# Kernel optimization log

Measured on AMD Instinct MI355X. Metric: run time of the kernel, lower is better.

## Reference

```python
import jax, jax.numpy as jnp
import numpy as np

D_MODEL = 512
NUM_HEADS = 8
DEPTH = D_MODEL // NUM_HEADS


def setup_inputs() -> dict:
    key = jax.random.key(0)
    ks = jax.random.split(key, 12)
    B, S, D = 2, 4096, D_MODEL
    scale = 1.0 / np.sqrt(D)
    return {
        "q": jax.random.normal(ks[0], (B, S, D), jnp.float32),
        "k": jax.random.normal(ks[1], (B, S, D), jnp.float32),
        "v": jax.random.normal(ks[2], (B, S, D), jnp.float32),
        "mask": jnp.zeros((B, 1, 1, S), jnp.float32),
        "wq": jax.random.normal(ks[3], (D, D), jnp.float32) * scale,
        "bq": jnp.zeros((D,), jnp.float32),
        "wk": jax.random.normal(ks[4], (D, D), jnp.float32) * scale,
        "bk": jnp.zeros((D,), jnp.float32),
        "wv": jax.random.normal(ks[5], (D, D), jnp.float32) * scale,
        "bv": jnp.zeros((D,), jnp.float32),
        "wo": jax.random.normal(ks[6], (D, D), jnp.float32) * scale,
        "bo": jnp.zeros((D,), jnp.float32),
    }


def _split_heads(x):
    # [B, S, D] -> [B, H, S, depth]
    B, S, _ = x.shape
    return x.reshape(B, S, NUM_HEADS, DEPTH).transpose(0, 2, 1, 3)


def reference(q, k, v, mask, wq, bq, wk, bk, wv, bv, wo, bo):
    B, S, D = q.shape
    query = _split_heads(q @ wq + bq)   # [B,H,S,d]
    key = _split_heads(k @ wk + bk)
    value = _split_heads(v @ wv + bv)
    # NOTE: original module does NOT scale by 1/sqrt(depth)
    score = jnp.einsum("bhqd,bhkd->bhqk", query, key)
    score = score + mask * -1e9
    attn = jax.nn.softmax(score, axis=-1)
    out = jnp.einsum("bhqk,bhkd->bhqd", attn, value)  # [B,H,S,d]
    out = out.transpose(0, 2, 1, 3).reshape(B, S, D)
    return out @ wo + bo
```

## Files before the change

### kernel.cpp

```cpp
#include <hip/hip_runtime.h>

#define NH   8
#define DH   64
#define NB   2
#define SEQ  4096
#define DM   512
#define MR   (NB * SEQ)
#define LSTR 72
#define LOG2E 1.44269504089f
#define NSPL 2
#define KVS  (SEQ / NSPL)
#define RH   (NB * NH * SEQ)
#define PSTR 36

using f16x8 = __attribute__((ext_vector_type(8))) _Float16;
using f32x4 = __attribute__((ext_vector_type(4))) float;
using h2    = __attribute__((ext_vector_type(2))) _Float16;
#define MFMA16(a, b, c) __builtin_amdgcn_mfma_f32_16x16x32_f16(a, b, c, 0, 0, 0)

#if defined(__has_builtin) && __has_builtin(__builtin_amdgcn_exp2f)
#define EXP2(x) __builtin_amdgcn_exp2f(x)
#else
extern "C" __device__ float __ocml_native_exp2_f32(float);
#define EXP2(x) __ocml_native_exp2_f32(x)
#endif

__device__ __forceinline__ unsigned pk_f16(float a, float b) {
    typedef __fp16 fp16v2 __attribute__((ext_vector_type(2)));
    union { fp16v2 h; unsigned u; } c;
    c.h = __builtin_amdgcn_cvt_pkrtz(a, b);
    return c.u;
}
__device__ __forceinline__ float m3(float a, float b, float c) {
    return fmaxf(fmaxf(a, b), c);
}
__device__ __forceinline__ float dot2acc(unsigned u, float c) {
#if defined(__has_builtin) && __has_builtin(__builtin_amdgcn_fdot2)
    h2 a = __builtin_bit_cast(h2, u);
    h2 one = {(_Float16)1.f, (_Float16)1.f};
    return __builtin_amdgcn_fdot2(a, one, c, false);
#else
    h2 a = __builtin_bit_cast(h2, u);
    return c + (float)a[0] + (float)a[1];
#endif
}
__device__ __forceinline__ void async16(void* lds, const void* g) {
    __builtin_amdgcn_global_load_lds(
        (__attribute__((address_space(1))) void*)g,
        (__attribute__((address_space(3))) void*)lds, 16, 0, 0);
}

__global__ __launch_bounds__(256) void cvt_w(
    const float* __restrict__ w0, const float* __restrict__ w1,
    const float* __restrict__ w2, const float* __restrict__ w3,
    _Float16* __restrict__ Wt)
{
    __shared__ _Float16 T[64 * LSTR];
    const int z = blockIdx.z;
    const float* W = (z == 0) ? w0 : (z == 1 ? w1 : (z == 2 ? w2 : w3));
    _Float16* out = Wt + (size_t)z * DM * DM;
    const int t = threadIdx.x;
    const int k0 = blockIdx.x * 64, n0 = blockIdx.y * 64;
#pragma unroll
    for (int i = 0; i < 4; ++i) {
        const int kl  = i * 16 + (t >> 4);
        const int nl4 = (t & 15) * 4;
        float4 u = *(const float4*)(W + (size_t)(k0 + kl) * DM + n0 + nl4);
        T[(nl4 + 0) * LSTR + kl] = (_Float16)u.x;
        T[(nl4 + 1) * LSTR + kl] = (_Float16)u.y;
        T[(nl4 + 2) * LSTR + kl] = (_Float16)u.z;
        T[(nl4 + 3) * LSTR + kl] = (_Float16)u.w;
    }
    __syncthreads();
#pragma unroll
    for (int i = 0; i < 2; ++i) {
        const int nl = i * 32 + (t >> 3);
        const int kc = (t & 7) * 8;
        *(uint4*)(out + (size_t)(n0 + nl) * DM + k0 + kc) = *(const uint4*)&T[nl * LSTR + kc];
    }
}

__global__ __launch_bounds__(256) void maskprep(const float* __restrict__ mask,
                                                float* __restrict__ mw)
{
    const int i = blockIdx.x * 256 + threadIdx.x;
    mw[i] = mask[i] * (-1e9f * LOG2E);
}

__global__ __launch_bounds__(256) void cvt_qkv(
    const float* __restrict__ q, const float* __restrict__ k,
    const float* __restrict__ v,
    _Float16* __restrict__ Qo, _Float16* __restrict__ Ko, _Float16* __restrict__ Vo)
{
    const size_t PER = (size_t)MR * DM;
    size_t base = ((size_t)blockIdx.x * 256 + threadIdx.x) * 8;
    const int tz = (int)(base / PER);
    const size_t off = base % PER;
    const float* s = (tz == 0) ? q : (tz == 1 ? k : v);
    _Float16* d    = (tz == 0) ? Qo : (tz == 1 ? Ko : Vo);
    float4 a = *(const float4*)(s + off);
    float4 b = *(const float4*)(s + off + 4);
    uint4 p = make_uint4(pk_f16(a.x, a.y), pk_f16(a.z, a.w),
                         pk_f16(b.x, b.y), pk_f16(b.z, b.w));
    *(uint4*)(d + off) = p;
}

__global__ __launch_bounds__(256) void proj3(
    const _Float16* __restrict__ Qin, const _Float16* __restrict__ Kin,
    const _Float16* __restrict__ Vin, const _Float16* __restrict__ Wt,
    const float* __restrict__ bq, const float* __restrict__ bk,
    const float* __restrict__ bv,
    _Float16* __restrict__ Qo, _Float16* __restrict__ Ko,
    _Float16* __restrict__ VTo)
{
    __shared__ _Float16 Xs[2][128 * 64];
    __shared__ _Float16 Ws[2][64 * 64];

    const int z = blockIdx.z;
    const _Float16* X = (z == 0) ? Qin : (z == 1 ? Kin : Vin);
    const _Float16* W = Wt + (size_t)z * DM * DM;
    const float* bias = (z == 0) ? bq : (z == 1 ? bk : bv);
    const float scale = (z == 0) ? LOG2E : 1.0f;

    const int t = threadIdx.x;
    const int l = t & 63, w = t >> 6;
    const int m = l & 15, g = l >> 4;
    const int ms = m & 7;
    const int row0 = blockIdx.x * 128;
    const int col0 = blockIdx.y * 64;

    int xr[4], xsw[4];
#pragma unroll
    for (int i = 0; i < 4; ++i) {
        const int c = w * 256 + i * 64 + l;
        xr[i]  = c >> 3;
        xsw[i] = ((c & 7) ^ (xr[i] & 7)) * 8;
    }
    int wr[2], wsw[2];
#pragma unroll
    for (int i = 0; i < 2; ++i) {
        const int c = w * 128 + i * 64 + l;
        wr[i]  = c >> 3;
        wsw[i] = ((c & 7) ^ (wr[i] & 7)) * 8;
    }

#pragma unroll
    for (int i = 0; i < 4; ++i)
        async16(&Xs[0][(w * 256 + i * 64) * 8], X + (size_t)(row0 + xr[i]) * DM + xsw[i]);
#pragma unroll
    for (int i = 0; i < 2; ++i)
        async16(&Ws[0][(w * 128 + i * 64) * 8], W + (size_t)(col0 + wr[i]) * DM + wsw[i]);

    f32x4 acc[2][4] = {};

    for (int k0 = 0; k0 < DM; k0 += 64) {
        const int p = (k0 >> 6) & 1;
        __syncthreads();
        if (k0 + 64 < DM) {
            const int kn = k0 + 64;
#pragma unroll
            for (int i = 0; i < 4; ++i)
                async16(&Xs[p ^ 1][(w * 256 + i * 64) * 8],
                        X + (size_t)(row0 + xr[i]) * DM + kn + xsw[i]);
#pragma unroll
            for (int i = 0; i < 2; ++i)
                async16(&Ws[p ^ 1][(w * 128 + i * 64) * 8],
                        W + (size_t)(col0 + wr[i]) * DM + kn + wsw[i]);
        }
#pragma unroll
        for (int kk = 0; kk < 2; ++kk) {
            const int slot = ((kk * 4 + g) ^ ms) * 8;
            f16x8 a0 = *(const f16x8*)&Xs[p][(w * 32 + m) * 64 + slot];
            f16x8 a1 = *(const f16x8*)&Xs[p][(w * 32 + 16 + m) * 64 + slot];
#pragma unroll
            for (int ct = 0; ct < 4; ++ct) {
                f16x8 bf = *(const f16x8*)&Ws[p][(ct * 16 + m) * 64 + slot];
                acc[0][ct] = MFMA16(a0, bf, acc[0][ct]);
                acc[1][ct] = MFMA16(a1, bf, acc[1][ct]);
            }
        }
    }

    float bv4[4];
#pragma unroll
    for (int ct = 0; ct < 4; ++ct) bv4[ct] = bias[col0 + ct * 16 + m];

    if (z == 2) {
        __syncthreads();
        _Float16* T = &Xs[0][0];
#pragma unroll
        for (int rt = 0; rt < 2; ++rt)
#pragma unroll
            for (int reg = 0; reg < 4; ++reg) {
                const int s_l = w * 32 + rt * 16 + g * 4 + reg;
#pragma unroll
                for (int ct = 0; ct < 4; ++ct) {
                    const int d = ct * 16 + m;
                    T[d * 136 + s_l] = (_Float16)(acc[rt][ct][reg] + bv4[ct]);
                }
            }
        __syncthreads();
        const int bb = row0 >> 12;
        const int s0 = row0 & (SEQ - 1);
#pragma unroll
        for (int j = 0; j < 4; ++j) {
            const int c = j * 256 + t;
            const int d = c >> 4;
            const int sc = (c & 15) * 8;
            *(uint4*)(VTo + (((size_t)bb * NH + blockIdx.y) * DH + d) * SEQ + s0 + sc) =
                *(const uint4*)&T[d * 136 + sc];
        }
    } else {
        _Float16* out = (z == 0) ? Qo : Ko;
#pragma unroll
        for (int rt = 0; rt < 2; ++rt)
#pragma unroll
            for (int reg = 0; reg < 4; ++reg) {
                const int row = row0 + w * 32 + rt * 16 + g * 4 + reg;
                const int bb = row >> 12;
                const int s  = row & (SEQ - 1);
#pragma unroll
                for (int ct = 0; ct < 4; ++ct)
                    out[(((size_t)bb * NH + blockIdx.y) * SEQ + s) * DH + ct * 16 + m] =
                        (_Float16)(scale * (acc[rt][ct][reg] + bv4[ct]));
            }
    }
}

__global__ __launch_bounds__(256) void gemm_out(const _Float16* __restrict__ X,
                                                const _Float16* __restrict__ W,
                                                const float* __restrict__ bias,
                                                float* __restrict__ out)
{
    __shared__ _Float16 Xs[2][128 * 64];
    __shared__ _Float16 Ws[2][64 * 64];

    const int t = threadIdx.x;
    const int l = t & 63, w = t >> 6;
    const int m = l & 15, g = l >> 4;
    const int ms = m & 7;
    const int row0 = blockIdx.x * 128;
    const int col0 = blockIdx.y * 64;

    int xr[4], xsw[4];
#pragma unroll
    for (int i = 0; i < 4; ++i) {
        const int c = w * 256 + i * 64 + l;
        xr[i]  = c >> 3;
        xsw[i] = ((c & 7) ^ (xr[i] & 7)) * 8;
    }
    int wr[2], wsw[2];
#pragma unroll
    for (int i = 0; i < 2; ++i) {
        const int c = w * 128 + i * 64 + l;
        wr[i]  = c >> 3;
        wsw[i] = ((c & 7) ^ (wr[i] & 7)) * 8;
    }

#pragma unroll
    for (int i = 0; i < 4; ++i)
        async16(&Xs[0][(w * 256 + i * 64) * 8], X + (size_t)(row0 + xr[i]) * DM + xsw[i]);
#pragma unroll
    for (int i = 0; i < 2; ++i)
        async16(&Ws[0][(w * 128 + i * 64) * 8], W + (size_t)(col0 + wr[i]) * DM + wsw[i]);

    f32x4 acc[2][4] = {};

    for (int k0 = 0; k0 < DM; k0 += 64) {
        const int p = (k0 >> 6) & 1;
        __syncthreads();
        if (k0 + 64 < DM) {
            const int kn = k0 + 64;
#pragma unroll
            for (int i = 0; i < 4; ++i)
                async16(&Xs[p ^ 1][(w * 256 + i * 64) * 8],
                        X + (size_t)(row0 + xr[i]) * DM + kn + xsw[i]);
#pragma unroll
            for (int i = 0; i < 2; ++i)
                async16(&Ws[p ^ 1][(w * 128 + i * 64) * 8],
                        W + (size_t)(col0 + wr[i]) * DM + kn + wsw[i]);
        }
#pragma unroll
        for (int kk = 0; kk < 2; ++kk) {
            const int slot = ((kk * 4 + g) ^ ms) * 8;
            f16x8 a0 = *(const f16x8*)&Xs[p][(w * 32 + m) * 64 + slot];
            f16x8 a1 = *(const f16x8*)&Xs[p][(w * 32 + 16 + m) * 64 + slot];
#pragma unroll
            for (int ct = 0; ct < 4; ++ct) {
                f16x8 bf = *(const f16x8*)&Ws[p][(ct * 16 + m) * 64 + slot];
                acc[0][ct] = MFMA16(a0, bf, acc[0][ct]);
                acc[1][ct] = MFMA16(a1, bf, acc[1][ct]);
            }
        }
    }

    float bv4[4];
#pragma unroll
    for (int ct = 0; ct < 4; ++ct) bv4[ct] = bias[col0 + ct * 16 + m];

#pragma unroll
    for (int rt = 0; rt < 2; ++rt)
#pragma unroll
        for (int reg = 0; reg < 4; ++reg) {
            const int row = row0 + w * 32 + rt * 16 + g * 4 + reg;
#pragma unroll
            for (int ct = 0; ct < 4; ++ct)
                out[(size_t)row * DM + col0 + ct * 16 + m] = acc[rt][ct][reg] + bv4[ct];
        }
}

__global__ __launch_bounds__(256, 3) void flash_mfma(
    const _Float16* __restrict__ Q, const _Float16* __restrict__ K,
    const _Float16* __restrict__ VT, const float* __restrict__ mw,
    _Float16* __restrict__ Op, float* __restrict__ Ml)
{
    __shared__ _Float16 Ks [2][64 * 64];
    __shared__ _Float16 VTs[2][64 * 64];
    __shared__ unsigned Ps[4][32 * PSTR];

    const int t = threadIdx.x;
    const int l = t & 63, w = t >> 6;
    const int m = l & 15, g = l >> 4;
    const int bh = blockIdx.y;
    const int b  = bh >> 3;
    const int q0 = blockIdx.x * 128;
    const int z  = blockIdx.z;
    const int kb0 = z * KVS;

    const _Float16* Qh  = Q  + (size_t)bh * SEQ * DH;
    const _Float16* Kh  = K  + (size_t)bh * SEQ * DH;
    const _Float16* VTh = VT + (size_t)bh * DH * SEQ;
    const float* mwb = mw + (size_t)b * SEQ;

    const int c0 = w * 128 + l, c1 = c0 + 64;
    const int r0 = c0 >> 3,     r1 = c1 >> 3;
    const int cl0 = (c0 & 7) ^ (r0 & 7), cl1 = (c1 & 7) ^ (r1 & 7);
    const int    gK0 = r0 * DH + cl0 * 8, gK1 = r1 * DH + cl1 * 8;
    const size_t gV0 = (size_t)r0 * SEQ + cl0 * 8, gV1 = (size_t)r1 * SEQ + cl1 * 8;
    const int ldsA = w * 1024, ldsB = ldsA + 512;

    async16(&Ks[0][ldsA], Kh + (size_t)kb0 * DH + gK0);
    async16(&Ks[0][ldsB], Kh + (size_t)kb0 * DH + gK1);
    async16(&VTs[0][ldsA], VTh + kb0 + gV0);
    async16(&VTs[0][ldsB], VTh + kb0 + gV1);

    f16x8 qf[2][2];
#pragma unroll
    for (int h = 0; h < 2; ++h)
#pragma unroll
        for (int kk = 0; kk < 2; ++kk)
            qf[h][kk] = *(const f16x8*)(Qh + (size_t)(q0 + w * 32 + h * 16 + m) * DH +
                                        kk * 32 + g * 8);

    float m_r[2] = {-INFINITY, -INFINITY}, l_r[2] = {0.f, 0.f};
    f32x4 oacc[2][4] = {};

    unsigned* Pw = &Ps[w][0];
    const int ms = m & 7;

    for (int it = 0; it < KVS / 64; ++it) {
        const int t0 = kb0 + it * 64;
        const int p  = it & 1;
        __syncthreads();

        if (it + 1 < KVS / 64) {
            const int tn = t0 + 64;
            async16(&Ks[p ^ 1][ldsA], Kh + (size_t)tn * DH + gK0);
            async16(&Ks[p ^ 1][ldsB], Kh + (size_t)tn * DH + gK1);
            async16(&VTs[p ^ 1][ldsA], VTh + tn + gV0);
            async16(&VTs[p ^ 1][ldsB], VTh + tn + gV1);
        }

        f32x4 sacc[2][4];
#pragma unroll
        for (int kt = 0; kt < 4; ++kt) {
            const f32x4 mv = *(const f32x4*)&mwb[t0 + kt * 16 + g * 4];
            sacc[0][kt] = mv;
            sacc[1][kt] = mv;
        }
#pragma unroll
        for (int kk = 0; kk < 2; ++kk) {
            const int slot = ((kk * 4 + g) ^ ms) * 8;
#pragma unroll
            for (int kt = 0; kt < 4; ++kt) {
                f16x8 kf = *(const f16x8*)&Ks[p][(kt * 16 + m) * 64 + slot];
                sacc[0][kt] = MFMA16(kf, qf[0][kk], sacc[0][kt]);
                sacc[1][kt] = MFMA16(kf, qf[1][kk], sacc[1][kt]);
            }
        }

        float lmax[2];
#pragma unroll
        for (int h = 0; h < 2; ++h) {
            const float x0 = m3(sacc[h][0][0], sacc[h][0][1], sacc[h][0][2]);
            const float x1 = m3(sacc[h][0][3], sacc[h][1][0], sacc[h][1][1]);
            const float x2 = m3(sacc[h][1][2], sacc[h][1][3], sacc[h][2][0]);
            const float x3 = m3(sacc[h][2][1], sacc[h][2][2], sacc[h][2][3]);
            const float x4 = m3(sacc[h][3][0], sacc[h][3][1], sacc[h][3][2]);
            lmax[h] = fmaxf(m3(x0, x1, x2), m3(x3, x4, sacc[h][3][3]));
        }

        if (!__all(lmax[0] <= m_r[0] + 8.f && lmax[1] <= m_r[1] + 8.f)) {
#pragma unroll
            for (int h = 0; h < 2; ++h) {
                float r = fmaxf(lmax[h], __shfl_xor(lmax[h], 16));
                r = fmaxf(r, __shfl_xor(r, 32));
                const float mnew  = fmaxf(m_r[h], r);
                const float alpha = EXP2(m_r[h] - mnew);
                m_r[h] = mnew;
                l_r[h] *= alpha;
#pragma unroll
                for (int dt = 0; dt < 4; ++dt)
#pragma unroll
                    for (int r4 = 0; r4 < 4; ++r4) oacc[h][dt][r4] *= alpha;
            }
        }

#pragma unroll
        for (int h = 0; h < 2; ++h) {
            const int pwr = (h * 16 + m) * PSTR + g * 2;
            float ps0 = 0.f, ps1 = 0.f;
#pragma unroll
            for (int kt = 0; kt < 4; ++kt) {
                const float p0 = EXP2(sacc[h][kt][0] - m_r[h]);
                const float p1 = EXP2(sacc[h][kt][1] - m_r[h]);
                const float p2 = EXP2(sacc[h][kt][2] - m_r[h]);
                const float p3 = EXP2(sacc[h][kt][3] - m_r[h]);
                const unsigned u0 = pk_f16(p0, p1);
                const unsigned u1 = pk_f16(p2, p3);
                *(uint2*)&Pw[pwr + kt * 8] = make_uint2(u0, u1);
                if (kt < 2) {
                    ps0 = dot2acc(u0, ps0);
                    ps0 = dot2acc(u1, ps0);
                } else {
                    ps1 = dot2acc(u0, ps1);
                    ps1 = dot2acc(u1, ps1);
                }
            }
            l_r[h] += ps0 + ps1;
        }

#pragma unroll
        for (int kk = 0; kk < 2; ++kk) {
            union { uint4 u4; f16x8 h; } pf[2];
#pragma unroll
            for (int h = 0; h < 2; ++h)
                pf[h].u4 = *(const uint4*)&Pw[(h * 16 + m) * PSTR + kk * 16 + g * 4];
            const int slot = ((kk * 4 + g) ^ ms) * 8;
#pragma unroll
            for (int dt = 0; dt < 4; ++dt) {
                f16x8 vf = *(const f16x8*)&VTs[p][(dt * 16 + m) * 64 + slot];
                oacc[0][dt] = MFMA16(vf, pf[0].h, oacc[0][dt]);
                oacc[1][dt] = MFMA16(vf, pf[1].h, oacc[1][dt]);
            }
        }
    }

#pragma unroll
    for (int h = 0; h < 2; ++h) {
        float lv = l_r[h];
        lv += __shfl_xor(lv, 16);
        lv += __shfl_xor(lv, 32);
        const float inv = 1.0f / lv;
        const int q = q0 + w * 32 + h * 16 + m;
        const size_t rowi = ((size_t)z * NB * NH + bh) * SEQ + q;
        _Float16* Orow = Op + rowi * DH;
#pragma unroll
        for (int dt = 0; dt < 4; ++dt) {
            _Float16 o4[4] = { (_Float16)(oacc[h][dt][0] * inv),
                               (_Float16)(oacc[h][dt][1] * inv),
                               (_Float16)(oacc[h][dt][2] * inv),
                               (_Float16)(oacc[h][dt][3] * inv) };
            *(uint2*)(Orow + dt * 16 + g * 4) = *(const uint2*)o4;
        }
        if (g == 0) ((float2*)Ml)[rowi] = make_float2(m_r[h], lv);
    }
}

__global__ __launch_bounds__(256) void combine(const _Float16* __restrict__ Op,
                                               const float* __restrict__ Ml,
                                               _Float16* __restrict__ O)
{
    const int i = blockIdx.x * 256 + threadIdx.x;
    const int r = i >> 4;
    const int dq = (i & 15) * 4;
    const float2 ml0 = ((const float2*)Ml)[r];
    const float2 ml1 = ((const float2*)Ml)[RH + r];
    const float M = fmaxf(ml0.x, ml1.x);
    float a0 = EXP2(ml0.x - M) * ml0.y;
    float a1 = EXP2(ml1.x - M) * ml1.y;
    const float inv = 1.f / (a0 + a1);
    a0 *= inv; a1 *= inv;
    union { uint2 u; _Float16 h[4]; } v0, v1, o;
    v0.u = *(const uint2*)(Op + (size_t)r * DH + dq);
    v1.u = *(const uint2*)(Op + ((size_t)RH + r) * DH + dq);
#pragma unroll
    for (int j = 0; j < 4; ++j)
        o.h[j] = (_Float16)(a0 * (float)v0.h[j] + a1 * (float)v1.h[j]);
    const int bh = r >> 12, q = r & (SEQ - 1);
    const int b = bh >> 3, h = bh & 7;
    *(uint2*)(O + ((size_t)b * SEQ + q) * DM + h * DH + dq) = o.u;
}

extern "C" void kernel_launch(void* const* d_in, const int* in_sizes, int n_in,
                              void* d_out, int out_size, void* d_ws, size_t ws_size,
                              hipStream_t stream) {
    const float* q    = (const float*)d_in[0];
    const float* k    = (const float*)d_in[1];
    const float* v    = (const float*)d_in[2];
    const float* mask = (const float*)d_in[3];
    const float* wq   = (const float*)d_in[4];
    const float* bq   = (const float*)d_in[5];
    const float* wk   = (const float*)d_in[6];
    const float* bk   = (const float*)d_in[7];
    const float* wv   = (const float*)d_in[8];
    const float* bv   = (const float*)d_in[9];
    const float* wo   = (const float*)d_in[10];
    const float* bo   = (const float*)d_in[11];

    const size_t P8 = (size_t)MR * DM;
    _Float16* Wt  = (_Float16*)d_ws;
    float*    mw  = (float*)(Wt + (size_t)4 * DM * DM);
    _Float16* Qin = (_Float16*)(mw + NB * SEQ);
    _Float16* Kin = Qin + P8;
    _Float16* Vin = Kin + P8;
    _Float16* Qws = Vin + P8;
    _Float16* Kws = Qws + P8;
    _Float16* VTws = Kws + P8;
    _Float16* Ows  = VTws + P8;

    _Float16* Opart = Qin;
    float*    Mlb   = (float*)Vin;

    cvt_w<<<dim3(8, 8, 4), 256, 0, stream>>>(wq, wk, wv, wo, Wt);
    maskprep<<<dim3(NB * SEQ / 256), 256, 0, stream>>>(mask, mw);
    cvt_qkv<<<dim3(3 * (MR * DM / 8) / 256), 256, 0, stream>>>(q, k, v, Qin, Kin, Vin);

    proj3<<<dim3(MR / 128, DM / 64, 3), 256, 0, stream>>>(
        Qin, Kin, Vin, Wt, bq, bk, bv, Qws, Kws, VTws);

    flash_mfma<<<dim3(SEQ / 128, NB * NH, NSPL), 256, 0, stream>>>(
        Qws, Kws, VTws, mw, Opart, Mlb);

    combine<<<dim3(RH * 16 / 256), 256, 0, stream>>>(Opart, Mlb, Ows);

    gemm_out<<<dim3(MR / 128, DM / 64), 256, 0, stream>>>(
        Ows, Wt + (size_t)3 * DM * DM, bo, (float*)d_out);
}
```

Baseline: 260.8 us.

## Remap flash block indices for XCD locality and prefetch mask one tile ahead

```diff
diff --git a/kernel.cpp b/kernel.cpp
--- a/kernel.cpp
+++ b/kernel.cpp
@@ -321,10 +321,13 @@
     const int t = threadIdx.x;
     const int l = t & 63, w = t >> 6;
     const int m = l & 15, g = l >> 4;
-    const int bh = blockIdx.y;
+
+    const unsigned wfl = blockIdx.x + 32u * blockIdx.y + 512u * blockIdx.z;
+    const unsigned o   = (wfl & 7u) * 128u + (wfl >> 3);
+    const int q0 = (int)(o & 31u) * 128;
+    const int bh = (int)(o >> 5) & 15;
+    const int z  = (int)(o >> 9);
     const int b  = bh >> 3;
-    const int q0 = blockIdx.x * 128;
-    const int z  = blockIdx.z;
     const int kb0 = z * KVS;
 
     const _Float16* Qh  = Q  + (size_t)bh * SEQ * DH;
@@ -352,6 +355,11 @@
             qf[h][kk] = *(const f16x8*)(Qh + (size_t)(q0 + w * 32 + h * 16 + m) * DH +
                                         kk * 32 + g * 8);
 
+    f32x4 mv[4];
+#pragma unroll
+    for (int kt = 0; kt < 4; ++kt)
+        mv[kt] = *(const f32x4*)&mwb[kb0 + kt * 16 + g * 4];
+
     float m_r[2] = {-INFINITY, -INFINITY}, l_r[2] = {0.f, 0.f};
     f32x4 oacc[2][4] = {};
 
@@ -361,22 +369,26 @@
     for (int it = 0; it < KVS / 64; ++it) {
         const int t0 = kb0 + it * 64;
         const int p  = it & 1;
+        const bool more = (it + 1 < KVS / 64);
         __syncthreads();
 
-        if (it + 1 < KVS / 64) {
+        f32x4 mvn[4];
+        if (more) {
             const int tn = t0 + 64;
             async16(&Ks[p ^ 1][ldsA], Kh + (size_t)tn * DH + gK0);
             async16(&Ks[p ^ 1][ldsB], Kh + (size_t)tn * DH + gK1);
             async16(&VTs[p ^ 1][ldsA], VTh + tn + gV0);
             async16(&VTs[p ^ 1][ldsB], VTh + tn + gV1);
+#pragma unroll
+            for (int kt = 0; kt < 4; ++kt)
+                mvn[kt] = *(const f32x4*)&mwb[tn + kt * 16 + g * 4];
         }
 
         f32x4 sacc[2][4];
 #pragma unroll
         for (int kt = 0; kt < 4; ++kt) {
-            const f32x4 mv = *(const f32x4*)&mwb[t0 + kt * 16 + g * 4];
-            sacc[0][kt] = mv;
-            sacc[1][kt] = mv;
+            sacc[0][kt] = mv[kt];
+            sacc[1][kt] = mv[kt];
         }
 #pragma unroll
         for (int kk = 0; kk < 2; ++kk) {
@@ -419,13 +431,15 @@
 #pragma unroll
         for (int h = 0; h < 2; ++h) {
             const int pwr = (h * 16 + m) * PSTR + g * 2;
+            const f32x4 mh = {m_r[h], m_r[h], m_r[h], m_r[h]};
             float ps0 = 0.f, ps1 = 0.f;
 #pragma unroll
             for (int kt = 0; kt < 4; ++kt) {
-                const float p0 = EXP2(sacc[h][kt][0] - m_r[h]);
-                const float p1 = EXP2(sacc[h][kt][1] - m_r[h]);
-                const float p2 = EXP2(sacc[h][kt][2] - m_r[h]);
-                const float p3 = EXP2(sacc[h][kt][3] - m_r[h]);
+                const f32x4 d = sacc[h][kt] - mh;
+                const float p0 = EXP2(d[0]);
+                const float p1 = EXP2(d[1]);
+                const float p2 = EXP2(d[2]);
+                const float p3 = EXP2(d[3]);
                 const unsigned u0 = pk_f16(p0, p1);
                 const unsigned u1 = pk_f16(p2, p3);
                 *(uint2*)&Pw[pwr + kt * 8] = make_uint2(u0, u1);
@@ -453,6 +467,11 @@
                 oacc[0][dt] = MFMA16(vf, pf[0].h, oacc[0][dt]);
                 oacc[1][dt] = MFMA16(vf, pf[1].h, oacc[1][dt]);
             }
+        }
+
+        if (more) {
+#pragma unroll
+            for (int kt = 0; kt < 4; ++kt) mv[kt] = mvn[kt];
         }
     }
 
```

After: 250.3 us. 4.0% less time.
